# Optimization experiments

Measured on AMD Instinct MI355X. Metric: run time of the kernel, lower is better.

The kernel has to match this reference:

```python
import jax, jax.numpy as jnp
import numpy as np

D_MODEL = 1024
N_HEAD = 16
HEAD_DIM = D_MODEL // N_HEAD
B, S = 4, 2048


def setup_inputs() -> dict:
    key = jax.random.key(0)
    ks = jax.random.split(key, 11)
    scale = 1.0 / np.sqrt(D_MODEL)
    inp = {
        "q": jax.random.normal(ks[0], (B, S, D_MODEL), jnp.float32),
        "k": jax.random.normal(ks[1], (B, S, D_MODEL), jnp.float32),
        "v": jax.random.normal(ks[2], (B, S, D_MODEL), jnp.float32),
        # torch nn.Linear weights: [out_features, in_features], y = x @ W.T + b
        "Wq": jax.random.normal(ks[3], (D_MODEL, D_MODEL), jnp.float32) * scale,
        "bq": jax.random.normal(ks[4], (D_MODEL,), jnp.float32) * scale,
        "Wk": jax.random.normal(ks[5], (D_MODEL, D_MODEL), jnp.float32) * scale,
        "bk": jax.random.normal(ks[6], (D_MODEL,), jnp.float32) * scale,
        "Wv": jax.random.normal(ks[7], (D_MODEL, D_MODEL), jnp.float32) * scale,
        "bv": jax.random.normal(ks[8], (D_MODEL,), jnp.float32) * scale,
        "Wo": jax.random.normal(ks[9], (D_MODEL, D_MODEL), jnp.float32) * scale,
        "bo": jax.random.normal(ks[10], (D_MODEL,), jnp.float32) * scale,
    }
    return inp


def _split_heads(x):
    # [B, S, D] -> [B, H, S, hd]
    b, s, _ = x.shape
    return x.reshape(b, s, N_HEAD, HEAD_DIM).transpose(0, 2, 1, 3)


def reference(q, k, v, Wq, bq, Wk, bk, Wv, bv, Wo, bo):
    qh = _split_heads(q @ Wq.T + bq)
    kh = _split_heads(k @ Wk.T + bk)
    vh = _split_heads(v @ Wv.T + bv)
    scores = jnp.einsum("bhqd,bhkd->bhqk", qh, kh) / jnp.sqrt(
        jnp.asarray(HEAD_DIM, qh.dtype)
    )
    weights = jax.nn.softmax(scores, axis=-1)  # [B, H, Sq, Sk]
    ctx = jnp.einsum("bhqk,bhkd->bhqd", weights, vh)
    b, h, s, d = ctx.shape
    ctx = ctx.transpose(0, 2, 1, 3).reshape(b, s, h * d)  # [B, S, D]
    return ctx @ Wo.T + bo
```

## Files before the change

kernel.cpp:

```cpp
#include <hip/hip_runtime.h>
#include <hip/hip_bf16.h>

typedef float   f32x4   __attribute__((ext_vector_type(4)));
typedef __bf16  bf16x8  __attribute__((ext_vector_type(8)));
typedef unsigned short u16x8 __attribute__((ext_vector_type(8)));
typedef unsigned short u16x4 __attribute__((ext_vector_type(4)));

#define DEVI __device__ __forceinline__

DEVI unsigned short f2bf_bits(float f) {
    __bf16 h = (__bf16)f;
    return __builtin_bit_cast(unsigned short, h);
}

DEVI f32x4 mfma_bf16(bf16x8 a, bf16x8 b, f32x4 c) {
    return __builtin_amdgcn_mfma_f32_16x16x32_bf16(a, b, c, 0, 0, 0);
}

template <bool A_F32, bool OUT_F32>
__global__ __launch_bounds__(256) void gemm_bt_kernel(
    const void* __restrict__ Ap, const float* __restrict__ W,
    const float* __restrict__ bias, void* __restrict__ Cp,
    int M, int N, int K, float scale)
{
    __shared__ __align__(16) char ldsA[128 * 128];
    __shared__ __align__(16) char ldsB[128 * 128];
    const int t = threadIdx.x;
    const int wave = t >> 6, lane = t & 63;
    const int g = lane >> 4, c = lane & 15;
    const int rowbase = blockIdx.x * 128;
    const int colbase = blockIdx.y * 128;
    const int wr = (wave >> 1) * 64, wc = (wave & 1) * 64;

    f32x4 acc[4][4] = {};

    for (int kt = 0; kt < K; kt += 64) {
#pragma unroll
        for (int ch = 0; ch < 4; ++ch) {
            int id = ch * 256 + t;
            int row = id >> 3;
            int col = (id & 7) * 8;
            int dst = row * 128 + ((col * 2) ^ ((row & 7) << 4));
            u16x8 hv;
            if constexpr (A_F32) {
                const float* src = (const float*)Ap + (size_t)(rowbase + row) * K + kt + col;
                f32x4 x0 = *(const f32x4*)src;
                f32x4 x1 = *(const f32x4*)(src + 4);
#pragma unroll
                for (int j = 0; j < 4; ++j) { hv[j] = f2bf_bits(x0[j]); hv[4 + j] = f2bf_bits(x1[j]); }
            } else {
                const unsigned short* src = (const unsigned short*)Ap + (size_t)(rowbase + row) * K + kt + col;
                hv = *(const u16x8*)src;
            }
            *(u16x8*)(ldsA + dst) = hv;

            const float* srcb = W + (size_t)(colbase + row) * K + kt + col;
            f32x4 y0 = *(const f32x4*)srcb;
            f32x4 y1 = *(const f32x4*)(srcb + 4);
            u16x8 hb;
#pragma unroll
            for (int j = 0; j < 4; ++j) { hb[j] = f2bf_bits(y0[j]); hb[4 + j] = f2bf_bits(y1[j]); }
            *(u16x8*)(ldsB + dst) = hb;
        }
        __syncthreads();

#pragma unroll
        for (int kk = 0; kk < 2; ++kk) {
            bf16x8 af[4], bfr[4];
#pragma unroll
            for (int i = 0; i < 4; ++i) {
                int ra = wr + i * 16 + c;
                af[i] = *(const bf16x8*)(ldsA + ra * 128 + ((kk * 64 + g * 16) ^ ((ra & 7) << 4)));
                int rb = wc + i * 16 + c;
                bfr[i] = *(const bf16x8*)(ldsB + rb * 128 + ((kk * 64 + g * 16) ^ ((rb & 7) << 4)));
            }
#pragma unroll
            for (int i = 0; i < 4; ++i)
#pragma unroll
                for (int j = 0; j < 4; ++j)
                    acc[i][j] = mfma_bf16(af[i], bfr[j], acc[i][j]);
        }
        __syncthreads();
    }

#pragma unroll
    for (int j = 0; j < 4; ++j) {
        int coln = colbase + wc + j * 16 + c;
        float bv = bias[coln];
#pragma unroll
        for (int i = 0; i < 4; ++i) {
            int row0 = rowbase + wr + i * 16 + g * 4;
#pragma unroll
            for (int r = 0; r < 4; ++r) {
                float val = (acc[i][j][r] + bv) * scale;
                if constexpr (OUT_F32)
                    ((float*)Cp)[(size_t)(row0 + r) * N + coln] = val;
                else
                    ((unsigned short*)Cp)[(size_t)(row0 + r) * N + coln] = f2bf_bits(val);
            }
        }
    }
}

__global__ __launch_bounds__(256) void transpose_v_kernel(
    const unsigned short* __restrict__ Vp, unsigned short* __restrict__ Vt)
{
    __shared__ unsigned short tile[64][72];
    const int t = threadIdx.x;
    const int bh = blockIdx.y, b = bh >> 4, h = bh & 15;
    const int s0 = blockIdx.x * 64;
#pragma unroll
    for (int ch = 0; ch < 2; ++ch) {
        int id = ch * 256 + t;
        int srow = id >> 3, dcol = (id & 7) * 8;
        u16x8 v = *(const u16x8*)(Vp + (size_t)(b * 2048 + s0 + srow) * 1024 + h * 64 + dcol);
        *(u16x8*)&tile[srow][dcol] = v;
    }
    __syncthreads();
#pragma unroll
    for (int ch = 0; ch < 2; ++ch) {
        int id = ch * 256 + t;
        int drow = id >> 3, scol = (id & 7) * 8;
        u16x8 ov;
#pragma unroll
        for (int j = 0; j < 8; ++j) ov[j] = tile[scol + j][drow];
        *(u16x8*)(Vt + (size_t)(bh * 64 + drow) * 2048 + s0 + scol) = ov;
    }
}

__global__ __launch_bounds__(256) void attn_kernel(
    const unsigned short* __restrict__ Qp, const unsigned short* __restrict__ Kp,
    const unsigned short* __restrict__ Vt, unsigned short* __restrict__ ctx)
{
    __shared__ __align__(16) char ldsK[64 * 128];
    __shared__ __align__(16) char ldsV[64 * 128];
    __shared__ __align__(16) char ldsP[4][2][16 * 128];
    const int t = threadIdx.x;
    const int wave = t >> 6, lane = t & 63;
    const int g = lane >> 4, c = lane & 15;
    const int bh = blockIdx.y, b = bh >> 4, h = bh & 15;
    const int qb = blockIdx.x * 128;

    bf16x8 qf0[2], qf1[2];
    {
        const unsigned short* q0 = Qp + (size_t)(b * 2048 + qb + wave * 32 + c) * 1024 + h * 64;
        qf0[0] = *(const bf16x8*)(q0 + 8 * g);
        qf0[1] = *(const bf16x8*)(q0 + 32 + 8 * g);
        const unsigned short* q1 = q0 + (size_t)16 * 1024;
        qf1[0] = *(const bf16x8*)(q1 + 8 * g);
        qf1[1] = *(const bf16x8*)(q1 + 32 + 8 * g);
    }

    f32x4 o0[4] = {}, o1[4] = {};
    float psum0 = 0.f, psum1 = 0.f;

    const int row0 = t >> 3, colB = (t & 7) * 8;
    const int row1 = 32 + row0;
    const int dst0 = row0 * 128 + ((colB * 2) ^ ((row0 & 7) << 4));
    const int dst1 = row1 * 128 + ((colB * 2) ^ ((row1 & 7) << 4));
    const unsigned short* Ksrc = Kp + (size_t)(b * 2048) * 1024 + h * 64;
    const unsigned short* Vsrc = Vt + (size_t)(bh * 64) * 2048;

    u16x8 kv0 = *(const u16x8*)(Ksrc + (size_t)row0 * 1024 + colB);
    u16x8 kv1 = *(const u16x8*)(Ksrc + (size_t)row1 * 1024 + colB);
    u16x8 vv0 = *(const u16x8*)(Vsrc + (size_t)row0 * 2048 + colB);
    u16x8 vv1 = *(const u16x8*)(Vsrc + (size_t)row1 * 2048 + colB);

    char* pw0 = ldsP[wave][0];
    char* pw1 = ldsP[wave][1];

    for (int kb = 0; kb < 2048; kb += 64) {
        *(u16x8*)(ldsK + dst0) = kv0;
        *(u16x8*)(ldsK + dst1) = kv1;
        *(u16x8*)(ldsV + dst0) = vv0;
        *(u16x8*)(ldsV + dst1) = vv1;
        __syncthreads();

        if (kb + 64 < 2048) {
            kv0 = *(const u16x8*)(Ksrc + (size_t)(kb + 64 + row0) * 1024 + colB);
            kv1 = *(const u16x8*)(Ksrc + (size_t)(kb + 64 + row1) * 1024 + colB);
            vv0 = *(const u16x8*)(Vsrc + (size_t)row0 * 2048 + kb + 64 + colB);
            vv1 = *(const u16x8*)(Vsrc + (size_t)row1 * 2048 + kb + 64 + colB);
        }

        f32x4 s0[4] = {}, s1[4] = {};
#pragma unroll
        for (int kk = 0; kk < 2; ++kk) {
            bf16x8 kf[4];
#pragma unroll
            for (int ti = 0; ti < 4; ++ti) {
                int rk = ti * 16 + c;
                kf[ti] = *(const bf16x8*)(ldsK + rk * 128 + ((kk * 64 + g * 16) ^ ((rk & 7) << 4)));
            }
#pragma unroll
            for (int ti = 0; ti < 4; ++ti) {
                s0[ti] = mfma_bf16(kf[ti], qf0[kk], s0[ti]);
                s1[ti] = mfma_bf16(kf[ti], qf1[kk], s1[ti]);
            }
        }

#pragma unroll
        for (int ti = 0; ti < 4; ++ti) {
            float p0 = __expf(s0[ti][0]);
            float p1 = __expf(s0[ti][1]);
            float p2 = __expf(s0[ti][2]);
            float p3 = __expf(s0[ti][3]);
            psum0 += (p0 + p1) + (p2 + p3);
            u16x4 hp;
            hp[0] = f2bf_bits(p0); hp[1] = f2bf_bits(p1);
            hp[2] = f2bf_bits(p2); hp[3] = f2bf_bits(p3);
            *(u16x4*)(pw0 + c * 128 + ((ti * 32 + g * 8) ^ ((c & 7) << 4))) = hp;
        }
#pragma unroll
        for (int ti = 0; ti < 4; ++ti) {
            float p0 = __expf(s1[ti][0]);
            float p1 = __expf(s1[ti][1]);
            float p2 = __expf(s1[ti][2]);
            float p3 = __expf(s1[ti][3]);
            psum1 += (p0 + p1) + (p2 + p3);
            u16x4 hp;
            hp[0] = f2bf_bits(p0); hp[1] = f2bf_bits(p1);
            hp[2] = f2bf_bits(p2); hp[3] = f2bf_bits(p3);
            *(u16x4*)(pw1 + c * 128 + ((ti * 32 + g * 8) ^ ((c & 7) << 4))) = hp;
        }

#pragma unroll
        for (int kk = 0; kk < 2; ++kk) {
            bf16x8 vf[4];
#pragma unroll
            for (int ti = 0; ti < 4; ++ti) {
                int rv = ti * 16 + c;
                vf[ti] = *(const bf16x8*)(ldsV + rv * 128 + ((kk * 64 + g * 16) ^ ((rv & 7) << 4)));
            }
            bf16x8 pa0 = *(const bf16x8*)(pw0 + c * 128 + ((kk * 64 + g * 16) ^ ((c & 7) << 4)));
            bf16x8 pa1 = *(const bf16x8*)(pw1 + c * 128 + ((kk * 64 + g * 16) ^ ((c & 7) << 4)));
#pragma unroll
            for (int ti = 0; ti < 4; ++ti) {
                o0[ti] = mfma_bf16(pa0, vf[ti], o0[ti]);
                o1[ti] = mfma_bf16(pa1, vf[ti], o1[ti]);
            }
        }
        __syncthreads();
    }

    psum0 += __shfl_xor(psum0, 16);
    psum0 += __shfl_xor(psum0, 32);
    psum1 += __shfl_xor(psum1, 16);
    psum1 += __shfl_xor(psum1, 32);

#pragma unroll
    for (int r = 0; r < 4; ++r) {
        float inv0 = 1.0f / __shfl(psum0, 4 * g + r);
        float inv1 = 1.0f / __shfl(psum1, 4 * g + r);
        int row0q = qb + wave * 32 + 4 * g + r;
        int row1q = row0q + 16;
#pragma unroll
        for (int ti = 0; ti < 4; ++ti) {
            int col = h * 64 + ti * 16 + c;
            ctx[(size_t)(b * 2048 + row0q) * 1024 + col] = f2bf_bits(o0[ti][r] * inv0);
            ctx[(size_t)(b * 2048 + row1q) * 1024 + col] = f2bf_bits(o1[ti][r] * inv1);
        }
    }
}

extern "C" void kernel_launch(void* const* d_in, const int* in_sizes, int n_in,
                              void* d_out, int out_size, void* d_ws, size_t ws_size,
                              hipStream_t stream)
{
    const float* q  = (const float*)d_in[0];
    const float* k  = (const float*)d_in[1];
    const float* v  = (const float*)d_in[2];
    const float* Wq = (const float*)d_in[3];
    const float* bq = (const float*)d_in[4];
    const float* Wk = (const float*)d_in[5];
    const float* bk = (const float*)d_in[6];
    const float* Wv = (const float*)d_in[7];
    const float* bv = (const float*)d_in[8];
    const float* Wo = (const float*)d_in[9];
    const float* bo = (const float*)d_in[10];
    float* out = (float*)d_out;

    char* ws = (char*)d_ws;
    const size_t SZ = (size_t)8192 * 1024 * 2;
    unsigned short* Qp = (unsigned short*)(ws);
    unsigned short* Kp = (unsigned short*)(ws + SZ);
    unsigned short* Vp = (unsigned short*)(ws + 2 * SZ);
    unsigned short* Vt = (unsigned short*)(ws + 3 * SZ);
    unsigned short* ctx = Vp;

    dim3 gg(64, 8);
    gemm_bt_kernel<true, false><<<gg, 256, 0, stream>>>(q, Wq, bq, Qp, 8192, 1024, 1024, 0.125f);
    gemm_bt_kernel<true, false><<<gg, 256, 0, stream>>>(k, Wk, bk, Kp, 8192, 1024, 1024, 1.0f);
    gemm_bt_kernel<true, false><<<gg, 256, 0, stream>>>(v, Wv, bv, Vp, 8192, 1024, 1024, 1.0f);
    transpose_v_kernel<<<dim3(32, 64), 256, 0, stream>>>(Vp, Vt);
    attn_kernel<<<dim3(16, 64), 256, 0, stream>>>(Qp, Kp, Vt, ctx);
    gemm_bt_kernel<false, true><<<gg, 256, 0, stream>>>(ctx, Wo, bo, out, 8192, 1024, 1024, 1.0f);
}
```

Baseline: 244.0 us.

## Fuse QKV projections into one launch, use exp2 softmax, raise MFMA priority

After: 289.1 us. 1.19x slower.

```diff
diff --git a/kernel.cpp b/kernel.cpp
--- a/kernel.cpp
+++ b/kernel.cpp
@@ -15,6 +15,93 @@
 
 DEVI f32x4 mfma_bf16(bf16x8 a, bf16x8 b, f32x4 c) {
     return __builtin_amdgcn_mfma_f32_16x16x32_bf16(a, b, c, 0, 0, 0);
+}
+
+__global__ __launch_bounds__(256) void qkv_proj_kernel(
+    const float* __restrict__ q, const float* __restrict__ k, const float* __restrict__ v,
+    const float* __restrict__ Wq, const float* __restrict__ Wk, const float* __restrict__ Wv,
+    const float* __restrict__ bq, const float* __restrict__ bk, const float* __restrict__ bv,
+    unsigned short* __restrict__ Qp, unsigned short* __restrict__ Kp, unsigned short* __restrict__ Vp)
+{
+    __shared__ __align__(16) char ldsA[128 * 128];
+    __shared__ __align__(16) char ldsB[128 * 128];
+    const int bid = blockIdx.x;
+    const int proj = bid >> 9;
+    const int rr = bid & 511;
+    const int rowbase = (rr >> 3) * 128;
+    const int colbase = (rr & 7) * 128;
+
+    const float* A    = proj == 0 ? q  : (proj == 1 ? k  : v);
+    const float* W    = proj == 0 ? Wq : (proj == 1 ? Wk : Wv);
+    const float* bias = proj == 0 ? bq : (proj == 1 ? bk : bv);
+    unsigned short* C = proj == 0 ? Qp : (proj == 1 ? Kp : Vp);
+    const float scale = proj == 0 ? 0.1803368801111244f : 1.0f;
+
+    const int t = threadIdx.x;
+    const int wave = t >> 6, lane = t & 63;
+    const int g = lane >> 4, c = lane & 15;
+    const int wr = (wave >> 1) * 64, wc = (wave & 1) * 64;
+
+    f32x4 acc[4][4] = {};
+
+    for (int kt = 0; kt < 1024; kt += 64) {
+#pragma unroll
+        for (int ch = 0; ch < 4; ++ch) {
+            int id = ch * 256 + t;
+            int row = id >> 3;
+            int col = (id & 7) * 8;
+            int dst = row * 128 + ((col * 2) ^ ((row & 7) << 4));
+            const float* src = A + (size_t)(rowbase + row) * 1024 + kt + col;
+            f32x4 x0 = *(const f32x4*)src;
+            f32x4 x1 = *(const f32x4*)(src + 4);
+            u16x8 hv;
+#pragma unroll
+            for (int j = 0; j < 4; ++j) { hv[j] = f2bf_bits(x0[j]); hv[4 + j] = f2bf_bits(x1[j]); }
+            *(u16x8*)(ldsA + dst) = hv;
+
+            const float* srcb = W + (size_t)(colbase + row) * 1024 + kt + col;
+            f32x4 y0 = *(const f32x4*)srcb;
+            f32x4 y1 = *(const f32x4*)(srcb + 4);
+            u16x8 hb;
+#pragma unroll
+            for (int j = 0; j < 4; ++j) { hb[j] = f2bf_bits(y0[j]); hb[4 + j] = f2bf_bits(y1[j]); }
+            *(u16x8*)(ldsB + dst) = hb;
+        }
+        __syncthreads();
+
+#pragma unroll
+        for (int kk = 0; kk < 2; ++kk) {
+            bf16x8 af[4], bfr[4];
+#pragma unroll
+            for (int i = 0; i < 4; ++i) {
+                int ra = wr + i * 16 + c;
+                af[i] = *(const bf16x8*)(ldsA + ra * 128 + ((kk * 64 + g * 16) ^ ((ra & 7) << 4)));
+                int rb = wc + i * 16 + c;
+                bfr[i] = *(const bf16x8*)(ldsB + rb * 128 + ((kk * 64 + g * 16) ^ ((rb & 7) << 4)));
+            }
+#pragma unroll
+            for (int i = 0; i < 4; ++i)
+#pragma unroll
+                for (int j = 0; j < 4; ++j)
+                    acc[i][j] = mfma_bf16(af[i], bfr[j], acc[i][j]);
+        }
+        __syncthreads();
+    }
+
+#pragma unroll
+    for (int j = 0; j < 4; ++j) {
+        int coln = colbase + wc + j * 16 + c;
+        float bv = bias[coln];
+#pragma unroll
+        for (int i = 0; i < 4; ++i) {
+            int row0 = rowbase + wr + i * 16 + g * 4;
+#pragma unroll
+            for (int r = 0; r < 4; ++r) {
+                float val = (acc[i][j][r] + bv) * scale;
+                C[(size_t)(row0 + r) * 1024 + coln] = f2bf_bits(val);
+            }
+        }
+    }
 }
 
 template <bool A_F32, bool OUT_F32>
@@ -192,19 +279,21 @@
                 int rk = ti * 16 + c;
                 kf[ti] = *(const bf16x8*)(ldsK + rk * 128 + ((kk * 64 + g * 16) ^ ((rk & 7) << 4)));
             }
+            __builtin_amdgcn_s_setprio(1);
 #pragma unroll
             for (int ti = 0; ti < 4; ++ti) {
                 s0[ti] = mfma_bf16(kf[ti], qf0[kk], s0[ti]);
                 s1[ti] = mfma_bf16(kf[ti], qf1[kk], s1[ti]);
             }
+            __builtin_amdgcn_s_setprio(0);
         }
 
 #pragma unroll
         for (int ti = 0; ti < 4; ++ti) {
-            float p0 = __expf(s0[ti][0]);
-            float p1 = __expf(s0[ti][1]);
-            float p2 = __expf(s0[ti][2]);
-            float p3 = __expf(s0[ti][3]);
+            float p0 = exp2f(s0[ti][0]);
+            float p1 = exp2f(s0[ti][1]);
+            float p2 = exp2f(s0[ti][2]);
+            float p3 = exp2f(s0[ti][3]);
             psum0 += (p0 + p1) + (p2 + p3);
             u16x4 hp;
             hp[0] = f2bf_bits(p0); hp[1] = f2bf_bits(p1);
@@ -213,10 +302,10 @@
         }
 #pragma unroll
         for (int ti = 0; ti < 4; ++ti) {
-            float p0 = __expf(s1[ti][0]);
-            float p1 = __expf(s1[ti][1]);
-            float p2 = __expf(s1[ti][2]);
-            float p3 = __expf(s1[ti][3]);
+            float p0 = exp2f(s1[ti][0]);
+            float p1 = exp2f(s1[ti][1]);
+            float p2 = exp2f(s1[ti][2]);
+            float p3 = exp2f(s1[ti][3]);
             psum1 += (p0 + p1) + (p2 + p3);
             u16x4 hp;
             hp[0] = f2bf_bits(p0); hp[1] = f2bf_bits(p1);
@@ -234,11 +323,13 @@
             }
             bf16x8 pa0 = *(const bf16x8*)(pw0 + c * 128 + ((kk * 64 + g * 16) ^ ((c & 7) << 4)));
             bf16x8 pa1 = *(const bf16x8*)(pw1 + c * 128 + ((kk * 64 + g * 16) ^ ((c & 7) << 4)));
+            __builtin_amdgcn_s_setprio(1);
 #pragma unroll
             for (int ti = 0; ti < 4; ++ti) {
                 o0[ti] = mfma_bf16(pa0, vf[ti], o0[ti]);
                 o1[ti] = mfma_bf16(pa1, vf[ti], o1[ti]);
             }
+            __builtin_amdgcn_s_setprio(0);
         }
         __syncthreads();
     }
@@ -288,11 +379,8 @@
     unsigned short* Vt = (unsigned short*)(ws + 3 * SZ);
     unsigned short* ctx = Vp;
 
-    dim3 gg(64, 8);
-    gemm_bt_kernel<true, false><<<gg, 256, 0, stream>>>(q, Wq, bq, Qp, 8192, 1024, 1024, 0.125f);
-    gemm_bt_kernel<true, false><<<gg, 256, 0, stream>>>(k, Wk, bk, Kp, 8192, 1024, 1024, 1.0f);
-    gemm_bt_kernel<true, false><<<gg, 256, 0, stream>>>(v, Wv, bv, Vp, 8192, 1024, 1024, 1.0f);
+    qkv_proj_kernel<<<dim3(1536), 256, 0, stream>>>(q, k, v, Wq, Wk, Wv, bq, bk, bv, Qp, Kp, Vp);
     transpose_v_kernel<<<dim3(32, 64), 256, 0, stream>>>(Vp, Vt);
     attn_kernel<<<dim3(16, 64), 256, 0, stream>>>(Qp, Kp, Vt, ctx);
-    gemm_bt_kernel<false, true><<<gg, 256, 0, stream>>>(ctx, Wo, bo, out, 8192, 1024, 1024, 1.0f);
-}
+    gemm_bt_kernel<false, true><<<dim3(64, 8), 256, 0, stream>>>(ctx, Wo, bo, out, 8192, 1024, 1024, 1.0f);
+}
```
